# Performance work log

Measured on AMD Instinct MI355X. Metric: run time of the kernel, lower is better.

Reference implementation:

```python
import jax, jax.numpy as jnp
import numpy as np

B, T, C, H = 2, 2048, 2048, 16
HD = C // H


def setup_inputs() -> dict:
    key = jax.random.key(0)
    ks = jax.random.split(key, 5)
    s = 0.02  # init scale for weights
    return {
        "x": jax.random.normal(ks[0], (B, T, C), jnp.float32),
        "Wq": jax.random.normal(ks[1], (C, C), jnp.float32) * s,
        "Wk": jax.random.normal(ks[2], (C, C), jnp.float32) * s,
        "Wv": jax.random.normal(ks[3], (C, C), jnp.float32) * s,
        "Wo": jax.random.normal(ks[4], (C, C), jnp.float32) * s,
        "bo": jnp.zeros((C,), jnp.float32),
    }


def _alibi_slopes(n_head):
    # power-of-2 path of _get_alibi_slopes (n_head=16 is a power of 2)
    return jnp.array([1.0 / 2 ** (i + 1) for i in range(n_head)], jnp.float32)


def reference(x, Wq, Wk, Wv, Wo, bo):
    b, t, c = x.shape
    h, hd = H, HD
    scale = 1.0 / np.sqrt(hd)
    # nn.Linear (no bias): y = x @ W.T; split heads -> (B,H,T,HD)
    q = (x @ Wq.T).reshape(b, t, h, hd).transpose(0, 2, 1, 3)
    k = (x @ Wk.T).reshape(b, t, h, hd).transpose(0, 2, 1, 3)
    v = (x @ Wv.T).reshape(b, t, h, hd).transpose(0, 2, 1, 3)
    scores = jnp.einsum("bhtd,bhsd->bhts", q, k) * scale  # (B,H,T,T)
    pos = jnp.arange(t)
    diff = pos[:, None] - pos[None, :]  # (T,T), i-j
    slopes = _alibi_slopes(h)
    bias = slopes[:, None, None] * diff.astype(jnp.float32)  # (H,T,T)
    causal = diff >= 0  # lower-triangular mask
    bias = jnp.where(causal[None, :, :], bias, -jnp.inf)
    scores = scores + bias[None]  # (B,H,T,T)
    attn = jax.nn.softmax(scores, axis=-1)  # dropout = identity (eval mode)
    out = jnp.einsum("bhts,bhsd->bhtd", attn, v)
    out = out.transpose(0, 2, 1, 3).reshape(b, t, c)
    out = out @ Wo.T + bo  # proj_dropout = identity (eval mode)
    return out, attn
```

## Files before the change

kernel.cpp:

```cpp
#include <hip/hip_runtime.h>
#include <hip/hip_bf16.h>

#define DEVINL __device__ __forceinline__

typedef __attribute__((ext_vector_type(8))) short bf16x8;
typedef __attribute__((ext_vector_type(4))) float f32x4;

DEVINL ushort f2bf(float f) {
  unsigned u = __float_as_uint(f);
  u += 0x7fffu + ((u >> 16) & 1u);
  return (ushort)(u >> 16);
}

DEVINL void gl_lds16(const void* g, void* lds) {
  __builtin_amdgcn_global_load_lds(
      (const __attribute__((address_space(1))) void*)g,
      (__attribute__((address_space(3))) void*)lds, 16, 0, 0);
}

DEVINL f32x4 mfma16(bf16x8 a, bf16x8 b, f32x4 c) {
  return __builtin_amdgcn_mfma_f32_16x16x32_bf16(a, b, c, 0, 0, 0);
}

__global__ __launch_bounds__(256) void cast_all_kernel(const float4* __restrict__ x,
                                                       const float4* __restrict__ wq,
                                                       const float4* __restrict__ wk,
                                                       const float4* __restrict__ wv,
                                                       const float4* __restrict__ wo,
                                                       ushort4* __restrict__ xb,
                                                       ushort4* __restrict__ wqb,
                                                       ushort4* __restrict__ wkb,
                                                       ushort4* __restrict__ wvb,
                                                       ushort4* __restrict__ wob) {
  const int blk = (int)blockIdx.x;
  const float4* src;
  ushort4* dst;
  int base;
  if (blk < 2048)      { src = x;  dst = xb;  base = blk; }
  else if (blk < 3072) { src = wq; dst = wqb; base = blk - 2048; }
  else if (blk < 4096) { src = wk; dst = wkb; base = blk - 3072; }
  else if (blk < 5120) { src = wv; dst = wvb; base = blk - 4096; }
  else                 { src = wo; dst = wob; base = blk - 5120; }
  const int idx0 = base * 1024 + (int)threadIdx.x;
#pragma unroll
  for (int i = 0; i < 4; ++i) {
    const int idx = idx0 + i * 256;
    float4 v = src[idx];
    dst[idx] = make_ushort4(f2bf(v.x), f2bf(v.y), f2bf(v.z), f2bf(v.w));
  }
}

template <int MODE>
__global__ __launch_bounds__(256) void gemm_nt(const ushort* __restrict__ A,
                                               const ushort* __restrict__ Bm,
                                               ushort* __restrict__ Qo,
                                               ushort* __restrict__ Ko,
                                               ushort* __restrict__ Vo,
                                               float* __restrict__ Fo,
                                               const float* __restrict__ bias,
                                               int M, int N, int K) {
  __shared__ __align__(16) ushort Al[2][8192];
  __shared__ __align__(16) ushort Bl[2][8192];
  const int tid = (int)threadIdx.x;
  const int l = tid & 63, w = tid >> 6;
  const int wr = w >> 1, wc = w & 1;
  const int lr = l & 15, lg = l >> 4;

  const int nwg = (int)(gridDim.x * gridDim.y);
  const int flat = (int)(blockIdx.y * gridDim.x + blockIdx.x);
  const int swz = (flat & 7) * (nwg >> 3) + (flat >> 3);
  const int bx = swz % (int)gridDim.x, by = swz / (int)gridDim.x;
  const int rowT = by * 128, colT = bx * 128;

  f32x4 acc[4][4] = {};

  auto stage = [&](int kt, int buf) {
#pragma unroll
    for (int q = 0; q < 4; ++q) {
      int s = q * 256 + tid;
      int rb = s >> 7, ks = (s >> 6) & 1, sl = s & 63;
      size_t koff = (size_t)(kt + ks * 32 + (sl >> 4) * 8);
      gl_lds16(A + (size_t)(rowT + rb * 16 + (sl & 15)) * K + koff,
               &Al[buf][(size_t)(q * 256 + (tid & 192)) * 8]);
      gl_lds16(Bm + (size_t)(colT + rb * 16 + (sl & 15)) * K + koff,
               &Bl[buf][(size_t)(q * 256 + (tid & 192)) * 8]);
    }
  };

  stage(0, 0);
  __syncthreads();
  int cur = 0;
  for (int kt = 0; kt < K; kt += 64) {
    if (kt + 64 < K) stage(kt + 64, cur ^ 1);
#pragma unroll
    for (int ks = 0; ks < 2; ++ks) {
      bf16x8 af[4], bfv[4];
#pragma unroll
      for (int i = 0; i < 4; ++i) {
        af[i]  = *(const bf16x8*)(&Al[cur][(((wr * 4 + i) * 2 + ks) * 64 + l) * 8]);
        bfv[i] = *(const bf16x8*)(&Bl[cur][(((wc * 4 + i) * 2 + ks) * 64 + l) * 8]);
      }
#pragma unroll
      for (int i = 0; i < 4; ++i)
#pragma unroll
        for (int j = 0; j < 4; ++j)
          acc[i][j] = mfma16(af[i], bfv[j], acc[i][j]);
    }
    __syncthreads();
    cur ^= 1;
  }

  const int seg = colT >> 11;
#pragma unroll
  for (int i = 0; i < 4; ++i) {
#pragma unroll
    for (int j = 0; j < 4; ++j) {
      const int col = colT + wc * 64 + j * 16 + lr;
#pragma unroll
      for (int e = 0; e < 4; ++e) {
        const int row = rowT + wr * 64 + i * 16 + lg * 4 + e;
        float v = acc[i][j][e];
        if (MODE == 3) {
          const int c = col & 2047;
          if (seg == 0)      Qo[(size_t)row * 2048 + c] = f2bf(v);
          else if (seg == 1) Ko[(size_t)row * 2048 + c] = f2bf(v);
          else               Vo[((size_t)((row >> 11) * 2048 + c)) * 2048 + (row & 2047)] = f2bf(v);
        } else {
          __builtin_nontemporal_store(v + bias[col], &Fo[(size_t)row * 2048 + col]);
        }
      }
    }
  }
}

__global__ __launch_bounds__(256) void flash_kernel(const ushort* __restrict__ Qg,
                                                    const ushort* __restrict__ Kg,
                                                    const ushort* __restrict__ Vt,
                                                    ushort* __restrict__ Og,
                                                    float2* __restrict__ stats) {
  __shared__ __align__(16) ushort Kl[2][8192];
  __shared__ __align__(16) ushort Vl[2][8192];
  __shared__ __align__(16) ushort Pl[4][1024];

  const int flat = (int)(blockIdx.y * gridDim.x + blockIdx.x);
  const int swz = (flat & 7) * 64 + (flat >> 3);
  const int bx = swz & 15, bh = swz >> 4;
  const int b = bh >> 4, h = bh & 15;
  const int tid = (int)threadIdx.x, l = tid & 63, w = tid >> 6;
  const int lr = l & 15, lg = l >> 4;
  const float scale = 0.08838834764831845f;
  const float slope = exp2f(-(float)(h + 1));
  const ushort* Kbase = Kg + ((size_t)b * 2048) * 2048 + h * 128;
  const ushort* Vbase = Vt + ((size_t)b * 2048 + h * 128) * 2048;

  for (int half = 0; half < 2; ++half) {
    const int qb = (half == 0) ? 31 - bx : bx;
    const int qr0 = qb * 64 + w * 16;

    bf16x8 qf[4];
#pragma unroll
    for (int ks = 0; ks < 4; ++ks)
      qf[ks] = *(const bf16x8*)(Qg + ((size_t)b * 2048 + qr0 + lr) * 2048 + h * 128 + ks * 32 + lg * 8);

    float runmax[4], runsum[4];
    f32x4 o[8] = {};
#pragma unroll
    for (int j = 0; j < 4; ++j) { runmax[j] = -__builtin_inff(); runsum[j] = 0.f; }

    auto stage = [&](int jt, int buf) {
#pragma unroll
      for (int q = 0; q < 4; ++q) {
        const int s = q * 256 + tid;
        const int sl = s & 63;
        const int cb = s >> 8, ks = (s >> 6) & 3;
        gl_lds16(Kbase + (size_t)(jt * 64 + cb * 16 + (sl & 15)) * 2048 + ks * 32 + (sl >> 4) * 8,
                 &Kl[buf][(size_t)(q * 256 + (tid & 192)) * 8]);
        const int db = s >> 7, k2 = (s >> 6) & 1;
        gl_lds16(Vbase + (size_t)(db * 16 + (sl & 15)) * 2048 + jt * 64 + k2 * 32 + (sl >> 4) * 8,
                 &Vl[buf][(size_t)(q * 256 + (tid & 192)) * 8]);
      }
    };

    stage(qb, 0);

    for (int jt = qb; jt >= 0; --jt) {
      const int cur = (qb - jt) & 1;
      if (jt > 0) {
        stage(jt - 1, cur ^ 1);
        asm volatile("s_waitcnt vmcnt(8)" ::: "memory");
      } else {
        asm volatile("s_waitcnt vmcnt(0)" ::: "memory");
      }
      __builtin_amdgcn_sched_barrier(0);
      __builtin_amdgcn_s_barrier();
      __builtin_amdgcn_sched_barrier(0);

      f32x4 sc[4];
      __builtin_amdgcn_s_setprio(1);
#pragma unroll
      for (int cb = 0; cb < 4; ++cb) {
        f32x4 a = {};
#pragma unroll
        for (int ks = 0; ks < 4; ++ks) {
          bf16x8 kf = *(const bf16x8*)(&Kl[cur][((cb * 4 + ks) * 64 + l) * 8]);
          a = mfma16(qf[ks], kf, a);
        }
        sc[cb] = a;
      }
      __builtin_amdgcn_s_setprio(0);
#pragma unroll
      for (int cb = 0; cb < 4; ++cb) {
        const int kj = jt * 64 + cb * 16 + lr;
#pragma unroll
        for (int j = 0; j < 4; ++j) {
          const int qi = qr0 + lg * 4 + j;
          sc[cb][j] = (kj <= qi) ? sc[cb][j] * scale + slope * (float)(qi - kj) : -__builtin_inff();
        }
      }

      float nm[4];
      bool need = false;
#pragma unroll
      for (int j = 0; j < 4; ++j) {
        float m = fmaxf(fmaxf(sc[0][j], sc[1][j]), fmaxf(sc[2][j], sc[3][j]));
#pragma unroll
        for (int d = 1; d < 16; d <<= 1) m = fmaxf(m, __shfl_xor(m, d));
        nm[j] = fmaxf(runmax[j], m);
        need = need || (nm[j] > runmax[j]);
      }
      if (__any(need)) {
#pragma unroll
        for (int j = 0; j < 4; ++j) {
          const float f = __expf(runmax[j] - nm[j]);
          runsum[j] *= f;
#pragma unroll
          for (int db = 0; db < 8; ++db) o[db][j] *= f;
          runmax[j] = nm[j];
        }
      }

#pragma unroll
      for (int cb = 0; cb < 4; ++cb) {
        const int kc = cb * 16 + lr;
#pragma unroll
        for (int j = 0; j < 4; ++j) {
          const float p = __expf(sc[cb][j] - runmax[j]);
          runsum[j] += p;
          const int l2 = (((kc & 31) >> 3) << 4) | (lg * 4 + j);
          Pl[w][((kc >> 5) * 64 + l2) * 8 + (kc & 7)] = f2bf(p);
        }
      }

      bf16x8 pf0 = *(const bf16x8*)(&Pl[w][(size_t)l * 8]);
      bf16x8 pf1 = *(const bf16x8*)(&Pl[w][(size_t)(64 + l) * 8]);
      __builtin_amdgcn_s_setprio(1);
#pragma unroll
      for (int db = 0; db < 8; ++db) {
        o[db] = mfma16(pf0, *(const bf16x8*)(&Vl[cur][((db * 2 + 0) * 64 + l) * 8]), o[db]);
        o[db] = mfma16(pf1, *(const bf16x8*)(&Vl[cur][((db * 2 + 1) * 64 + l) * 8]), o[db]);
      }
      __builtin_amdgcn_s_setprio(0);

      __builtin_amdgcn_sched_barrier(0);
      __builtin_amdgcn_s_barrier();
      __builtin_amdgcn_sched_barrier(0);
    }

#pragma unroll
    for (int j = 0; j < 4; ++j) {
      float s = runsum[j];
#pragma unroll
      for (int d = 1; d < 16; d <<= 1) s += __shfl_xor(s, d);
      const float iv = 1.0f / s;
      if (lr == 0) stats[(size_t)bh * 2048 + qr0 + lg * 4 + j] = make_float2(runmax[j], iv);
#pragma unroll
      for (int db = 0; db < 8; ++db) o[db][j] *= iv;
    }
#pragma unroll
    for (int db = 0; db < 8; ++db)
#pragma unroll
      for (int j = 0; j < 4; ++j)
        Og[((size_t)b * 2048 + qr0 + lg * 4 + j) * 2048 + h * 128 + db * 16 + lr] = f2bf(o[db][j]);
  }
}

__global__ __launch_bounds__(256) void probs_kernel(const ushort* __restrict__ Qg,
                                                    const ushort* __restrict__ Kg,
                                                    const float2* __restrict__ stats,
                                                    float* __restrict__ attn_out) {
  const int kb = (int)blockIdx.x, qb = (int)blockIdx.y, bh = (int)blockIdx.z;
  const int tid = (int)threadIdx.x;

  if (kb > qb) {
    float* base = attn_out + ((size_t)bh * 2048 + qb * 128) * 2048 + kb * 128;
    const f32x4 z = {0.f, 0.f, 0.f, 0.f};
#pragma unroll
    for (int it = 0; it < 16; ++it) {
      const int idx = it * 256 + tid;
      __builtin_nontemporal_store(z, (f32x4*)(base + (size_t)(idx >> 5) * 2048 + (idx & 31) * 4));
    }
    return;
  }

  __shared__ __align__(16) ushort Ql[16384];
  __shared__ __align__(16) ushort Kl[16384];
  const int b = bh >> 4, h = bh & 15;
  const int l = tid & 63, w = tid >> 6;
  const int wr = w >> 1, wc = w & 1;
  const int lr = l & 15, lg = l >> 4;
  const float scale = 0.08838834764831845f;
  const float slope = exp2f(-(float)(h + 1));

#pragma unroll
  for (int q = 0; q < 8; ++q) {
    const int s = q * 256 + tid;
    const int sl = s & 63, rb = s >> 8, ks = (s >> 6) & 3;
    const size_t koff = (size_t)(h * 128 + ks * 32 + (sl >> 4) * 8);
    gl_lds16(Qg + ((size_t)b * 2048 + qb * 128 + rb * 16 + (sl & 15)) * 2048 + koff,
             Ql + (size_t)(q * 256 + (tid & 192)) * 8);
    gl_lds16(Kg + ((size_t)b * 2048 + kb * 128 + rb * 16 + (sl & 15)) * 2048 + koff,
             Kl + (size_t)(q * 256 + (tid & 192)) * 8);
  }
  __syncthreads();

  f32x4 acc[4][4] = {};
#pragma unroll
  for (int ks = 0; ks < 4; ++ks) {
    bf16x8 af[4], bfv[4];
#pragma unroll
    for (int i = 0; i < 4; ++i) {
      af[i]  = *(const bf16x8*)(Ql + (((wr * 4 + i) * 4 + ks) * 64 + l) * 8);
      bfv[i] = *(const bf16x8*)(Kl + (((wc * 4 + i) * 4 + ks) * 64 + l) * 8);
    }
#pragma unroll
    for (int i = 0; i < 4; ++i)
#pragma unroll
      for (int j = 0; j < 4; ++j)
        acc[i][j] = mfma16(af[i], bfv[j], acc[i][j]);
  }

  float2 st[4][4];
#pragma unroll
  for (int i = 0; i < 4; ++i)
#pragma unroll
    for (int e = 0; e < 4; ++e)
      st[i][e] = stats[(size_t)bh * 2048 + qb * 128 + wr * 64 + i * 16 + lg * 4 + e];

#pragma unroll
  for (int i = 0; i < 4; ++i) {
#pragma unroll
    for (int j = 0; j < 4; ++j) {
      const int kj = kb * 128 + wc * 64 + j * 16 + lr;
#pragma unroll
      for (int e = 0; e < 4; ++e) {
        const int qi = qb * 128 + wr * 64 + i * 16 + lg * 4 + e;
        const float sv = acc[i][j][e] * scale + slope * (float)(qi - kj);
        float p = __expf(sv - st[i][e].x) * st[i][e].y;
        if (kj > qi) p = 0.f;
        __builtin_nontemporal_store(p, &attn_out[((size_t)bh * 2048 + qi) * 2048 + kj]);
      }
    }
  }
}

extern "C" void kernel_launch(void* const* d_in, const int* in_sizes, int n_in,
                              void* d_out, int out_size, void* d_ws, size_t ws_size,
                              hipStream_t stream) {
  (void)in_sizes; (void)n_in; (void)out_size; (void)ws_size;
  const float* x  = (const float*)d_in[0];
  const float* Wq = (const float*)d_in[1];
  const float* Wk = (const float*)d_in[2];
  const float* Wv = (const float*)d_in[3];
  const float* Wo = (const float*)d_in[4];
  const float* bo = (const float*)d_in[5];

  float* outp  = (float*)d_out;
  float* attnp = outp + (size_t)4096 * 2048;

  char* ws = (char*)d_ws;
  ushort* xb   = (ushort*)(ws);
  ushort* wqkv = (ushort*)(ws + (16ull << 20));
  ushort* wob  = (ushort*)(ws + (40ull << 20));
  ushort* Qb   = (ushort*)(ws + (48ull << 20));
  ushort* Kb   = (ushort*)(ws + (64ull << 20));
  ushort* Vtb  = (ushort*)(ws + (80ull << 20));
  ushort* Ob   = (ushort*)(ws + (96ull << 20));
  float2* stats = (float2*)(ws);

  cast_all_kernel<<<6144, 256, 0, stream>>>(
      (const float4*)x, (const float4*)Wq, (const float4*)Wk, (const float4*)Wv,
      (const float4*)Wo, (ushort4*)xb, (ushort4*)wqkv, (ushort4*)(wqkv + 4194304),
      (ushort4*)(wqkv + 2 * 4194304), (ushort4*)wob);

  gemm_nt<3><<<dim3(48, 32), 256, 0, stream>>>(xb, wqkv, Qb, Kb, Vtb, nullptr, nullptr,
                                               4096, 6144, 2048);

  flash_kernel<<<dim3(16, 32), 256, 0, stream>>>(Qb, Kb, Vtb, Ob, stats);
  probs_kernel<<<dim3(16, 16, 32), 256, 0, stream>>>(Qb, Kb, stats, attnp);

  gemm_nt<2><<<dim3(16, 32), 256, 0, stream>>>(Ob, wob, nullptr, nullptr, nullptr, outp, bo,
                                               4096, 2048, 2048);
}
```

Baseline: 523.8 us.

## Fuse output projection GEMM and attention-probs kernel into one tail launch

Merges the output-projection GEMM and the attention-probability materialization kernel into a single launch. The first 512 blocks run the projection GEMM and the remaining 8192 blocks compute or zero-fill the attn tiles, sharing one 64KB LDS buffer. The goal is to drop one launch and let the compute-bound GEMM overlap with the store-bound probs work instead of running them back to back. The catch is that block scheduling order decides how much they actually overlap, and the merged kernel carries the larger LDS footprint and register pressure of both paths.

```diff
diff --git a/kernel.cpp b/kernel.cpp
--- a/kernel.cpp
+++ b/kernel.cpp
@@ -50,15 +50,12 @@
   }
 }
 
-template <int MODE>
-__global__ __launch_bounds__(256) void gemm_nt(const ushort* __restrict__ A,
-                                               const ushort* __restrict__ Bm,
-                                               ushort* __restrict__ Qo,
-                                               ushort* __restrict__ Ko,
-                                               ushort* __restrict__ Vo,
-                                               float* __restrict__ Fo,
-                                               const float* __restrict__ bias,
-                                               int M, int N, int K) {
+__global__ __launch_bounds__(256) void gemm_qkv(const ushort* __restrict__ A,
+                                                const ushort* __restrict__ Bm,
+                                                ushort* __restrict__ Qo,
+                                                ushort* __restrict__ Ko,
+                                                ushort* __restrict__ Vo,
+                                                int M, int N, int K) {
   __shared__ __align__(16) ushort Al[2][8192];
   __shared__ __align__(16) ushort Bl[2][8192];
   const int tid = (int)threadIdx.x;
@@ -120,14 +117,10 @@
       for (int e = 0; e < 4; ++e) {
         const int row = rowT + wr * 64 + i * 16 + lg * 4 + e;
         float v = acc[i][j][e];
-        if (MODE == 3) {
-          const int c = col & 2047;
-          if (seg == 0)      Qo[(size_t)row * 2048 + c] = f2bf(v);
-          else if (seg == 1) Ko[(size_t)row * 2048 + c] = f2bf(v);
-          else               Vo[((size_t)((row >> 11) * 2048 + c)) * 2048 + (row & 2047)] = f2bf(v);
-        } else {
-          __builtin_nontemporal_store(v + bias[col], &Fo[(size_t)row * 2048 + col]);
-        }
+        const int c = col & 2047;
+        if (seg == 0)      Qo[(size_t)row * 2048 + c] = f2bf(v);
+        else if (seg == 1) Ko[(size_t)row * 2048 + c] = f2bf(v);
+        else               Vo[((size_t)((row >> 11) * 2048 + c)) * 2048 + (row & 2047)] = f2bf(v);
       }
     }
   }
@@ -284,12 +277,85 @@
   }
 }
 
-__global__ __launch_bounds__(256) void probs_kernel(const ushort* __restrict__ Qg,
-                                                    const ushort* __restrict__ Kg,
-                                                    const float2* __restrict__ stats,
-                                                    float* __restrict__ attn_out) {
-  const int kb = (int)blockIdx.x, qb = (int)blockIdx.y, bh = (int)blockIdx.z;
+__global__ __launch_bounds__(256) void tail_kernel(const ushort* __restrict__ Ob,
+                                                   const ushort* __restrict__ wob,
+                                                   float* __restrict__ outp,
+                                                   const float* __restrict__ bias,
+                                                   const ushort* __restrict__ Qg,
+                                                   const ushort* __restrict__ Kg,
+                                                   const float2* __restrict__ stats,
+                                                   float* __restrict__ attn_out) {
+  __shared__ __align__(16) ushort SM[32768];
+  const int blk = (int)blockIdx.x;
   const int tid = (int)threadIdx.x;
+  const int l = tid & 63, w = tid >> 6;
+  const int lr = l & 15, lg = l >> 4;
+
+  if (blk < 512) {
+    ushort (*Al)[8192] = (ushort(*)[8192])(SM);
+    ushort (*Bl)[8192] = (ushort(*)[8192])(SM + 16384);
+    const int wr = w >> 1, wc = w & 1;
+    const int swz = (blk & 7) * 64 + (blk >> 3);
+    const int bx = swz & 15, by = swz >> 4;
+    const int rowT = by * 128, colT = bx * 128;
+    const int K = 2048;
+
+    f32x4 acc[4][4] = {};
+
+    auto stage = [&](int kt, int buf) {
+#pragma unroll
+      for (int q = 0; q < 4; ++q) {
+        int s = q * 256 + tid;
+        int rb = s >> 7, ks = (s >> 6) & 1, sl = s & 63;
+        size_t koff = (size_t)(kt + ks * 32 + (sl >> 4) * 8);
+        gl_lds16(Ob + (size_t)(rowT + rb * 16 + (sl & 15)) * K + koff,
+                 &Al[buf][(size_t)(q * 256 + (tid & 192)) * 8]);
+        gl_lds16(wob + (size_t)(colT + rb * 16 + (sl & 15)) * K + koff,
+                 &Bl[buf][(size_t)(q * 256 + (tid & 192)) * 8]);
+      }
+    };
+
+    stage(0, 0);
+    __syncthreads();
+    int cur = 0;
+    for (int kt = 0; kt < K; kt += 64) {
+      if (kt + 64 < K) stage(kt + 64, cur ^ 1);
+#pragma unroll
+      for (int ks = 0; ks < 2; ++ks) {
+        bf16x8 af[4], bfv[4];
+#pragma unroll
+        for (int i = 0; i < 4; ++i) {
+          af[i]  = *(const bf16x8*)(&Al[cur][(((wr * 4 + i) * 2 + ks) * 64 + l) * 8]);
+          bfv[i] = *(const bf16x8*)(&Bl[cur][(((wc * 4 + i) * 2 + ks) * 64 + l) * 8]);
+        }
+#pragma unroll
+        for (int i = 0; i < 4; ++i)
+#pragma unroll
+          for (int j = 0; j < 4; ++j)
+            acc[i][j] = mfma16(af[i], bfv[j], acc[i][j]);
+      }
+      __syncthreads();
+      cur ^= 1;
+    }
+
+#pragma unroll
+    for (int i = 0; i < 4; ++i) {
+#pragma unroll
+      for (int j = 0; j < 4; ++j) {
+        const int col = colT + wc * 64 + j * 16 + lr;
+#pragma unroll
+        for (int e = 0; e < 4; ++e) {
+          const int row = rowT + wr * 64 + i * 16 + lg * 4 + e;
+          __builtin_nontemporal_store(acc[i][j][e] + bias[col],
+                                      &outp[(size_t)row * 2048 + col]);
+        }
+      }
+    }
+    return;
+  }
+
+  const int rem = blk - 512;
+  const int kb = rem & 15, qb = (rem >> 4) & 15, bh = rem >> 8;
 
   if (kb > qb) {
     float* base = attn_out + ((size_t)bh * 2048 + qb * 128) * 2048 + kb * 128;
@@ -302,12 +368,10 @@
     return;
   }
 
-  __shared__ __align__(16) ushort Ql[16384];
-  __shared__ __align__(16) ushort Kl[16384];
+  ushort* Ql = SM;
+  ushort* Kl = SM + 16384;
   const int b = bh >> 4, h = bh & 15;
-  const int l = tid & 63, w = tid >> 6;
   const int wr = w >> 1, wc = w & 1;
-  const int lr = l & 15, lg = l >> 4;
   const float scale = 0.08838834764831845f;
   const float slope = exp2f(-(float)(h + 1));
 
@@ -392,12 +456,9 @@
       (const float4*)Wo, (ushort4*)xb, (ushort4*)wqkv, (ushort4*)(wqkv + 4194304),
       (ushort4*)(wqkv + 2 * 4194304), (ushort4*)wob);
 
-  gemm_nt<3><<<dim3(48, 32), 256, 0, stream>>>(xb, wqkv, Qb, Kb, Vtb, nullptr, nullptr,
-                                               4096, 6144, 2048);
+  gemm_qkv<<<dim3(48, 32), 256, 0, stream>>>(xb, wqkv, Qb, Kb, Vtb, 4096, 6144, 2048);
 
   flash_kernel<<<dim3(16, 32), 256, 0, stream>>>(Qb, Kb, Vtb, Ob, stats);
-  probs_kernel<<<dim3(16, 16, 32), 256, 0, stream>>>(Qb, Kb, stats, attnp);
-
-  gemm_nt<2><<<dim3(16, 32), 256, 0, stream>>>(Ob, wob, nullptr, nullptr, nullptr, outp, bo,
-                                               4096, 2048, 2048);
-}
+
+  tail_kernel<<<8704, 256, 0, stream>>>(Ob, wob, outp, bo, Qb, Kb, stats, attnp);
+}
```

Result: no change. 518.8 us (-1.0%).
